# Optimization experiments

Measured on AMD Instinct MI355X. Metric: run time of the kernel, lower is better.

The kernel has to match this reference:

```python
import jax, jax.numpy as jnp
import numpy as np

N = 8192
IN_DIM = 128
THETA_DIM = 256
OUT_DIM = 64
BN_EPS = 1e-5
LEAKY_SLOPE = 0.01


def setup_inputs() -> dict:
    key = jax.random.key(0)
    ks = jax.random.split(key, 8)
    H = jax.random.normal(ks[0], (N, IN_DIM), dtype=jnp.float32)
    # fixed adjacency passed to __init__; nonnegative so mask=ceil(A*1e-5) is {0,1}
    A = jax.random.uniform(ks[1], (N, N), dtype=jnp.float32)
    bn_gamma = jnp.ones((IN_DIM,), dtype=jnp.float32)
    bn_beta = jnp.zeros((IN_DIM,), dtype=jnp.float32)
    W1 = jax.random.normal(ks[2], (IN_DIM, THETA_DIM), dtype=jnp.float32) / np.sqrt(IN_DIM)
    b1 = jnp.zeros((THETA_DIM,), dtype=jnp.float32)
    Wout = jax.random.normal(ks[3], (IN_DIM, OUT_DIM), dtype=jnp.float32) / np.sqrt(IN_DIM)
    bout = jnp.zeros((OUT_DIM,), dtype=jnp.float32)
    return {"H": H, "A": A, "bn_gamma": bn_gamma, "bn_beta": bn_beta,
            "W1": W1, "b1": b1, "Wout": Wout, "bout": bout}


def reference(H, A, bn_gamma, bn_beta, W1, b1, Wout, bout):
    # BatchNorm1d in training mode: batch stats over the N (node) axis, biased var
    mean = jnp.mean(H, axis=0)
    var = jnp.mean(jnp.square(H - mean), axis=0)
    Hn = (H - mean) * jax.lax.rsqrt(var + BN_EPS) * bn_gamma + bn_beta  # [N, IN_DIM]

    Hx = Hn @ W1 + b1                                    # [N, THETA_DIM]
    scores = jax.nn.sigmoid(Hx @ Hx.T)                   # [N, N]
    mask = jnp.ceil(A * 1e-5)                            # binary mask from fixed A
    n = A.shape[0]
    A1 = jnp.maximum(scores, 0.1) * mask + jnp.eye(n, dtype=H.dtype)  # [N, N]

    # D_hat @ A1 @ D_hat is just symmetric row/col scaling by deg^-0.5
    d = jnp.power(jnp.sum(A1, axis=1), -0.5)             # [N]
    A_hat = A1 * d[:, None] * d[None, :]                 # [N, N]

    out = A_hat @ (Hn @ Wout + bout)                     # [N, OUT_DIM]
    out = jnp.where(out >= 0, out, LEAKY_SLOPE * out)    # LeakyReLU(0.01)
    return out, A1
```

## Files before the change

kernel.cpp:

```cpp
#include <hip/hip_runtime.h>
#include <math.h>

#define NN 8192
#define IN_DIM 128
#define THETA_DIM 256
#define OUT_DIM 64

typedef _Float16 half_t;
typedef _Float16 f16x8 __attribute__((ext_vector_type(8)));
typedef _Float16 f16x4 __attribute__((ext_vector_type(4)));
typedef float f32x4 __attribute__((ext_vector_type(4)));

#define WS_SCALE 0
#define WS_SHIFT 128
#define WS_SUM   256
#define WS_SQ    384
#define WS_ROWSUM 512
#define WS_D     8704
#define WS_HN    16896
#define WS_HX    (WS_HN + NN*IN_DIM)
#define WS_Z     (WS_HX + NN*THETA_DIM)
#define WS_OBUF  (WS_Z + NN*OUT_DIM)
#define WS_ZDHT  (WS_OBUF + NN*OUT_DIM)
#define WS_MASK  (WS_ZDHT + NN*OUT_DIM/2)

__global__ __launch_bounds__(256) void k_zero(float* __restrict__ ws) {
    int b = blockIdx.x, tid = threadIdx.x;
    float4 z = (float4){0.f, 0.f, 0.f, 0.f};
    if (b < 9) {
        int i = b * 256 + tid;
        if (i < 2112) ((float4*)(ws + WS_SUM))[i] = z;
    } else {
        int i = (b - 9) * 256 + tid;
        ((float4*)(ws + WS_OBUF))[i] = z;
    }
}

__global__ __launch_bounds__(256) void k_stats(const float* __restrict__ H, float* __restrict__ ws) {
    int tid = threadIdx.x;
    int c = tid & 127, h = tid >> 7;
    int rb = blockIdx.x * 128;
    float s = 0.f, q = 0.f;
    for (int r = h; r < 128; r += 2) {
        float v = H[(size_t)(rb + r) * IN_DIM + c];
        s += v; q += v * v;
    }
    atomicAdd(&ws[WS_SUM + c], s);
    atomicAdd(&ws[WS_SQ + c], q);
}

__global__ void k_finalize(const float* __restrict__ gamma, const float* __restrict__ beta, float* __restrict__ ws) {
    int c = threadIdx.x;
    float mean = ws[WS_SUM + c] * (1.f / NN);
    float var  = ws[WS_SQ + c] * (1.f / NN) - mean * mean;
    float rstd = 1.f / sqrtf(var + 1e-5f);
    float sc = rstd * gamma[c];
    ws[WS_SCALE + c] = sc;
    ws[WS_SHIFT + c] = beta[c] - mean * sc;
}

__global__ __launch_bounds__(256) void k_hn(const float* __restrict__ H, const float* __restrict__ ws, float* __restrict__ Hn) {
    int i = blockIdx.x * 256 + threadIdx.x;
    const float4* H4 = (const float4*)H;
    float4 v = H4[i];
    int cb = (i & 31) * 4;
    float4 sc = *(const float4*)&ws[WS_SCALE + cb];
    float4 sh = *(const float4*)&ws[WS_SHIFT + cb];
    float4 o;
    o.x = v.x * sc.x + sh.x; o.y = v.y * sc.y + sh.y;
    o.z = v.z * sc.z + sh.z; o.w = v.w * sc.w + sh.w;
    ((float4*)Hn)[i] = o;
}

__global__ __launch_bounds__(256) void k_mask(const float* __restrict__ Amat, unsigned int* __restrict__ mask) {
    int idx = blockIdx.x * 256 + threadIdx.x;
    const float4* A4 = (const float4*)Amat;
#pragma unroll
    for (int it = 0; it < 4; it++) {
        int g = idx + it * 524288;
        unsigned int bits = 0u;
#pragma unroll
        for (int w = 0; w < 8; w++) {
            float4 a = A4[(size_t)g * 8 + w];
            bits |= (a.x > 0.f ? 1u : 0u) << (w * 4 + 0);
            bits |= (a.y > 0.f ? 1u : 0u) << (w * 4 + 1);
            bits |= (a.z > 0.f ? 1u : 0u) << (w * 4 + 2);
            bits |= (a.w > 0.f ? 1u : 0u) << (w * 4 + 3);
        }
        mask[g] = bits;
    }
}

__global__ __launch_bounds__(256) void k_hx(const float* __restrict__ Hn, const float* __restrict__ W1,
                                            const float* __restrict__ b1, half_t* __restrict__ Hx) {
    __shared__ float HnS[32 * IN_DIM];
    int tid = threadIdx.x;
    int row0 = blockIdx.x * 32;
    const float4* src = (const float4*)(Hn + (size_t)row0 * IN_DIM);
    float4* dst = (float4*)HnS;
#pragma unroll
    for (int q = 0; q < 4; q++) dst[q * 256 + tid] = src[q * 256 + tid];
    __syncthreads();
    int c = tid;
    float acc[32];
#pragma unroll
    for (int r = 0; r < 32; r++) acc[r] = 0.f;
    for (int k0 = 0; k0 < IN_DIM; k0 += 4) {
        float w0 = W1[(size_t)(k0 + 0) * THETA_DIM + c];
        float w1 = W1[(size_t)(k0 + 1) * THETA_DIM + c];
        float w2 = W1[(size_t)(k0 + 2) * THETA_DIM + c];
        float w3 = W1[(size_t)(k0 + 3) * THETA_DIM + c];
#pragma unroll
        for (int r = 0; r < 32; r++) {
            float4 h = *(const float4*)&HnS[r * IN_DIM + k0];
            acc[r] += h.x * w0 + h.y * w1 + h.z * w2 + h.w * w3;
        }
    }
    float bb = b1[c];
#pragma unroll
    for (int r = 0; r < 32; r++) Hx[(size_t)(row0 + r) * THETA_DIM + c] = (half_t)(acc[r] + bb);
}

__global__ __launch_bounds__(256) void k_y(const float* __restrict__ Hn, const float* __restrict__ Wout,
                                           const float* __restrict__ bout, float* __restrict__ Y) {
    __shared__ float HnS[64 * IN_DIM];
    int tid = threadIdx.x;
    int row0 = blockIdx.x * 64;
    const float4* src = (const float4*)(Hn + (size_t)row0 * IN_DIM);
    float4* dst = (float4*)HnS;
#pragma unroll
    for (int q = 0; q < 8; q++) dst[q * 256 + tid] = src[q * 256 + tid];
    __syncthreads();
    int c = tid & 63, rg = tid >> 6;
    float acc[16];
#pragma unroll
    for (int r = 0; r < 16; r++) acc[r] = 0.f;
    for (int k0 = 0; k0 < IN_DIM; k0 += 4) {
        float w0 = Wout[(size_t)(k0 + 0) * OUT_DIM + c];
        float w1 = Wout[(size_t)(k0 + 1) * OUT_DIM + c];
        float w2 = Wout[(size_t)(k0 + 2) * OUT_DIM + c];
        float w3 = Wout[(size_t)(k0 + 3) * OUT_DIM + c];
#pragma unroll
        for (int r = 0; r < 16; r++) {
            float4 h = *(const float4*)&HnS[(rg * 16 + r) * IN_DIM + k0];
            acc[r] += h.x * w0 + h.y * w1 + h.z * w2 + h.w * w3;
        }
    }
    float bb = bout[c];
#pragma unroll
    for (int r = 0; r < 16; r++) Y[(size_t)(row0 + rg * 16 + r) * OUT_DIM + c] = acc[r] + bb;
}

__global__ __launch_bounds__(256) void k_scores(const half_t* __restrict__ Hx,
                                                const unsigned char* __restrict__ mask,
                                                float* __restrict__ A1, float* __restrict__ rowsum) {
    __shared__ half_t Rs[128 * 72];
    __shared__ half_t Cs[128 * 72];
    int tid = threadIdx.x;
    int R = blockIdx.x * 128, C = blockIdx.y * 128;
    int lane = tid & 63, wv = tid >> 6;
    int li = lane & 15, lg = lane >> 4;
    int qi = (wv >> 1) * 64, qj = (wv & 1) * 64;
    int su = tid & 7;

    f32x4 acc[4][4];
#pragma unroll
    for (int t = 0; t < 4; t++)
#pragma unroll
        for (int u = 0; u < 4; u++) acc[t][u] = (f32x4){0.f, 0.f, 0.f, 0.f};

    f16x8 ra[4], rb[4];
#pragma unroll
    for (int q = 0; q < 4; q++) {
        int r = (q * 256 + tid) >> 3;
        ra[q] = *(const f16x8*)(Hx + (size_t)(R + r) * THETA_DIM + su * 8);
        rb[q] = *(const f16x8*)(Hx + (size_t)(C + r) * THETA_DIM + su * 8);
    }

    for (int s = 0; s < 4; s++) {
        __syncthreads();
#pragma unroll
        for (int q = 0; q < 4; q++) {
            int r = (q * 256 + tid) >> 3;
            *(f16x8*)(Rs + r * 72 + su * 8) = ra[q];
            *(f16x8*)(Cs + r * 72 + su * 8) = rb[q];
        }
        if (s < 3) {
            int k0 = (s + 1) * 64;
#pragma unroll
            for (int q = 0; q < 4; q++) {
                int r = (q * 256 + tid) >> 3;
                ra[q] = *(const f16x8*)(Hx + (size_t)(R + r) * THETA_DIM + k0 + su * 8);
                rb[q] = *(const f16x8*)(Hx + (size_t)(C + r) * THETA_DIM + k0 + su * 8);
            }
        }
        __syncthreads();
#pragma unroll
        for (int kk = 0; kk < 2; kk++) {
            f16x8 af[4], bf[4];
#pragma unroll
            for (int t = 0; t < 4; t++)
                af[t] = *(const f16x8*)(Cs + (qi + t * 16 + li) * 72 + kk * 32 + lg * 8);
#pragma unroll
            for (int u = 0; u < 4; u++)
                bf[u] = *(const f16x8*)(Rs + (qj + u * 16 + li) * 72 + kk * 32 + lg * 8);
#pragma unroll
            for (int t = 0; t < 4; t++)
#pragma unroll
                for (int u = 0; u < 4; u++)
                    acc[t][u] = __builtin_amdgcn_mfma_f32_16x16x32_f16(af[t], bf[u], acc[t][u], 0, 0, 0);
        }
    }

#pragma unroll
    for (int u = 0; u < 4; u++) {
        int gr = R + qj + u * 16 + li;
        unsigned long long m64 = *(const unsigned long long*)&mask[(size_t)gr * 1024 + ((C + qi) >> 3)];
        float rsum = 0.f;
#pragma unroll
        for (int t = 0; t < 4; t++) {
            int gc0 = C + qi + t * 16 + lg * 4;
            float4 wv4;
            float* pv = (float*)&wv4;
#pragma unroll
            for (int jj = 0; jj < 4; jj++) {
                float x = acc[t][u][jj];
                float sg = 1.f / (1.f + __expf(-x));
                float m = (float)((m64 >> (t * 16 + lg * 4 + jj)) & 1ULL);
                float v = fmaxf(sg, 0.1f) * m + ((gr == gc0 + jj) ? 1.f : 0.f);
                pv[jj] = v;
                rsum += v;
            }
            *(float4*)&A1[(size_t)gr * NN + gc0] = wv4;
        }
        rsum += __shfl_xor(rsum, 16, 64);
        rsum += __shfl_xor(rsum, 32, 64);
        if (lg == 0) atomicAdd(&rowsum[gr], rsum);
    }
}

__global__ void k_dvec(float* __restrict__ ws) {
    int i = blockIdx.x * 256 + threadIdx.x;
    ws[WS_D + i] = 1.f / sqrtf(ws[WS_ROWSUM + i]);
}

__global__ __launch_bounds__(256) void k_scalez(const float* __restrict__ dvec, const float* __restrict__ Z,
                                                half_t* __restrict__ ZdhT) {
    __shared__ float T[64 * 68];
    int tid = threadIdx.x;
    int j0 = blockIdx.x * 64;
#pragma unroll
    for (int q = 0; q < 4; q++) {
        int unit = q * 256 + tid;
        int j = unit >> 4, c4 = (unit & 15) * 4;
        float dj = dvec[j0 + j];
        float4 v = *(const float4*)&Z[(size_t)(j0 + j) * OUT_DIM + c4];
        v.x *= dj; v.y *= dj; v.z *= dj; v.w *= dj;
        *(float4*)&T[j * 68 + c4] = v;
    }
    __syncthreads();
#pragma unroll
    for (int q = 0; q < 2; q++) {
        int unit = q * 256 + tid;
        int c = unit >> 3, j8 = (unit & 7) * 8;
        f16x8 h;
#pragma unroll
        for (int x = 0; x < 8; x++) h[x] = (half_t)T[(j8 + x) * 68 + c];
        *(f16x8*)&ZdhT[(size_t)c * NN + j0 + j8] = h;
    }
}

__global__ __launch_bounds__(256) void k_spmm(const float* __restrict__ A1, const half_t* __restrict__ ZdhT,
                                              float* __restrict__ obuf) {
    __shared__ half_t As[128 * 72];
    __shared__ half_t Bs[64 * 72];
    int tid = threadIdx.x;
    int row0 = blockIdx.x * 128;
    int j0 = blockIdx.y * 512;
    int lane = tid & 63, wv = tid >> 6;
    int li = lane & 15, lg = lane >> 4;
    int ar = tid >> 4, ac4 = (tid & 15) * 4;
    int bn = tid >> 3, bk8 = (tid & 7) * 8;

    f32x4 acc[2][4];
#pragma unroll
    for (int t = 0; t < 2; t++)
#pragma unroll
        for (int u = 0; u < 4; u++) acc[t][u] = (f32x4){0.f, 0.f, 0.f, 0.f};

    float4 va[8];
    f16x8 vb[2];
#pragma unroll
    for (int q = 0; q < 8; q++)
        va[q] = *(const float4*)&A1[(size_t)(row0 + (q * 16 + ar)) * NN + j0 + ac4];
#pragma unroll
    for (int q = 0; q < 2; q++)
        vb[q] = *(const f16x8*)&ZdhT[(size_t)(q * 32 + bn) * NN + j0 + bk8];

    for (int jc = j0; jc < j0 + 512; jc += 64) {
        __syncthreads();
#pragma unroll
        for (int q = 0; q < 8; q++) {
            f16x4 h; h[0] = (half_t)va[q].x; h[1] = (half_t)va[q].y; h[2] = (half_t)va[q].z; h[3] = (half_t)va[q].w;
            *(f16x4*)&As[(q * 16 + ar) * 72 + ac4] = h;
        }
#pragma unroll
        for (int q = 0; q < 2; q++)
            *(f16x8*)&Bs[(q * 32 + bn) * 72 + bk8] = vb[q];
        if (jc + 64 < j0 + 512) {
#pragma unroll
            for (int q = 0; q < 8; q++)
                va[q] = *(const float4*)&A1[(size_t)(row0 + (q * 16 + ar)) * NN + jc + 64 + ac4];
#pragma unroll
            for (int q = 0; q < 2; q++)
                vb[q] = *(const f16x8*)&ZdhT[(size_t)(q * 32 + bn) * NN + jc + 64 + bk8];
        }
        __syncthreads();
#pragma unroll
        for (int kk = 0; kk < 2; kk++) {
            f16x8 af[2], bf[4];
#pragma unroll
            for (int t = 0; t < 2; t++)
                af[t] = *(const f16x8*)&As[(wv * 32 + t * 16 + li) * 72 + kk * 32 + lg * 8];
#pragma unroll
            for (int u = 0; u < 4; u++)
                bf[u] = *(const f16x8*)&Bs[(u * 16 + li) * 72 + kk * 32 + lg * 8];
#pragma unroll
            for (int t = 0; t < 2; t++)
#pragma unroll
                for (int u = 0; u < 4; u++)
                    acc[t][u] = __builtin_amdgcn_mfma_f32_16x16x32_f16(af[t], bf[u], acc[t][u], 0, 0, 0);
        }
    }
#pragma unroll
    for (int t = 0; t < 2; t++)
#pragma unroll
        for (int u = 0; u < 4; u++)
#pragma unroll
            for (int r = 0; r < 4; r++)
                atomicAdd(&obuf[(size_t)(row0 + wv * 32 + t * 16 + lg * 4 + r) * OUT_DIM + u * 16 + li],
                          acc[t][u][r]);
}

__global__ void k_out(const float* __restrict__ ws, float* __restrict__ out) {
    int i = blockIdx.x * 256 + threadIdx.x;
    const float4* O4 = (const float4*)(ws + WS_OBUF);
    int row = i >> 4;
    float d = ws[WS_D + row];
    float4 v = O4[i];
    float a = d * v.x, b = d * v.y, cc = d * v.z, e = d * v.w;
    v.x = (a >= 0.f) ? a : 0.01f * a;
    v.y = (b >= 0.f) ? b : 0.01f * b;
    v.z = (cc >= 0.f) ? cc : 0.01f * cc;
    v.w = (e >= 0.f) ? e : 0.01f * e;
    ((float4*)out)[i] = v;
}

extern "C" void kernel_launch(void* const* d_in, const int* in_sizes, int n_in,
                              void* d_out, int out_size, void* d_ws, size_t ws_size,
                              hipStream_t stream) {
    const float* H     = (const float*)d_in[0];
    const float* A     = (const float*)d_in[1];
    const float* gamma = (const float*)d_in[2];
    const float* beta  = (const float*)d_in[3];
    const float* W1    = (const float*)d_in[4];
    const float* b1    = (const float*)d_in[5];
    const float* Wout  = (const float*)d_in[6];
    const float* bout  = (const float*)d_in[7];
    float* out = (float*)d_out;
    float* A1  = out + (size_t)NN * OUT_DIM;
    float* ws  = (float*)d_ws;
    half_t* Hx = (half_t*)(ws + WS_HX);
    half_t* ZdhT = (half_t*)(ws + WS_ZDHT);
    unsigned int* maskw = (unsigned int*)(ws + WS_MASK);

    k_zero<<<521, 256, 0, stream>>>(ws);
    k_mask<<<2048, 256, 0, stream>>>(A, maskw);
    k_stats<<<64, 256, 0, stream>>>(H, ws);
    k_finalize<<<1, 128, 0, stream>>>(gamma, beta, ws);
    k_hn<<<1024, 256, 0, stream>>>(H, ws, ws + WS_HN);
    k_hx<<<256, 256, 0, stream>>>(ws + WS_HN, W1, b1, Hx);
    k_y<<<128, 256, 0, stream>>>(ws + WS_HN, Wout, bout, ws + WS_Z);
    dim3 g6(64, 64);
    k_scores<<<g6, 256, 0, stream>>>(Hx, (const unsigned char*)maskw, A1, ws + WS_ROWSUM);
    k_dvec<<<32, 256, 0, stream>>>(ws);
    k_scalez<<<128, 256, 0, stream>>>(ws + WS_D, ws + WS_Z, ZdhT);
    k_spmm<<<dim3(64, 16), 256, 0, stream>>>(A1, ZdhT, ws + WS_OBUF);
    k_out<<<512, 256, 0, stream>>>(ws, out);
}
```

Baseline: 337.8 us.

## Restructure spmm with direct-register A loads, partial buffers, and nontemporal traffic

k_spmm now loads A1 rows straight into registers in MFMA fragment layout instead of staging them through shared memory, and double-buffers the Z tile in LDS so there is one barrier per step. Its float atomics on the output are replaced by per-split partial buffers that a new output kernel sums before scaling and applying LeakyReLU, so the zeroing of the output buffer is dropped. Nontemporal loads and stores are added for the large A and A1 streams, the mask prefetch in k_scores is hoisted before the main loop, and k_stats gets more blocks. The partial buffers cost extra workspace and extra read traffic in the final kernel.

```diff
diff --git a/kernel.cpp b/kernel.cpp
--- a/kernel.cpp
+++ b/kernel.cpp
@@ -23,25 +23,19 @@
 #define WS_OBUF  (WS_Z + NN*OUT_DIM)
 #define WS_ZDHT  (WS_OBUF + NN*OUT_DIM)
 #define WS_MASK  (WS_ZDHT + NN*OUT_DIM/2)
+#define WS_OBUFP (WS_MASK + NN*(NN/32))
 
 __global__ __launch_bounds__(256) void k_zero(float* __restrict__ ws) {
-    int b = blockIdx.x, tid = threadIdx.x;
-    float4 z = (float4){0.f, 0.f, 0.f, 0.f};
-    if (b < 9) {
-        int i = b * 256 + tid;
-        if (i < 2112) ((float4*)(ws + WS_SUM))[i] = z;
-    } else {
-        int i = (b - 9) * 256 + tid;
-        ((float4*)(ws + WS_OBUF))[i] = z;
-    }
+    int i = blockIdx.x * 256 + threadIdx.x;
+    if (i < 2112) ((float4*)(ws + WS_SUM))[i] = (float4){0.f, 0.f, 0.f, 0.f};
 }
 
 __global__ __launch_bounds__(256) void k_stats(const float* __restrict__ H, float* __restrict__ ws) {
     int tid = threadIdx.x;
     int c = tid & 127, h = tid >> 7;
-    int rb = blockIdx.x * 128;
+    int rb = blockIdx.x * 32;
     float s = 0.f, q = 0.f;
-    for (int r = h; r < 128; r += 2) {
+    for (int r = h; r < 32; r += 2) {
         float v = H[(size_t)(rb + r) * IN_DIM + c];
         s += v; q += v * v;
     }
@@ -74,18 +68,18 @@
 
 __global__ __launch_bounds__(256) void k_mask(const float* __restrict__ Amat, unsigned int* __restrict__ mask) {
     int idx = blockIdx.x * 256 + threadIdx.x;
-    const float4* A4 = (const float4*)Amat;
+    const f32x4* A4 = (const f32x4*)Amat;
 #pragma unroll
     for (int it = 0; it < 4; it++) {
         int g = idx + it * 524288;
         unsigned int bits = 0u;
 #pragma unroll
         for (int w = 0; w < 8; w++) {
-            float4 a = A4[(size_t)g * 8 + w];
-            bits |= (a.x > 0.f ? 1u : 0u) << (w * 4 + 0);
-            bits |= (a.y > 0.f ? 1u : 0u) << (w * 4 + 1);
-            bits |= (a.z > 0.f ? 1u : 0u) << (w * 4 + 2);
-            bits |= (a.w > 0.f ? 1u : 0u) << (w * 4 + 3);
+            f32x4 a = __builtin_nontemporal_load(&A4[(size_t)g * 8 + w]);
+            bits |= (a[0] > 0.f ? 1u : 0u) << (w * 4 + 0);
+            bits |= (a[1] > 0.f ? 1u : 0u) << (w * 4 + 1);
+            bits |= (a[2] > 0.f ? 1u : 0u) << (w * 4 + 2);
+            bits |= (a[3] > 0.f ? 1u : 0u) << (w * 4 + 3);
         }
         mask[g] = bits;
     }
@@ -176,6 +170,12 @@
         ra[q] = *(const f16x8*)(Hx + (size_t)(R + r) * THETA_DIM + su * 8);
         rb[q] = *(const f16x8*)(Hx + (size_t)(C + r) * THETA_DIM + su * 8);
     }
+    unsigned long long m64p[4];
+#pragma unroll
+    for (int u = 0; u < 4; u++) {
+        int gr = R + qj + u * 16 + li;
+        m64p[u] = *(const unsigned long long*)&mask[(size_t)gr * 1024 + ((C + qi) >> 3)];
+    }
 
     for (int s = 0; s < 4; s++) {
         __syncthreads();
@@ -215,23 +215,22 @@
 #pragma unroll
     for (int u = 0; u < 4; u++) {
         int gr = R + qj + u * 16 + li;
-        unsigned long long m64 = *(const unsigned long long*)&mask[(size_t)gr * 1024 + ((C + qi) >> 3)];
+        unsigned long long m64 = m64p[u];
         float rsum = 0.f;
 #pragma unroll
         for (int t = 0; t < 4; t++) {
             int gc0 = C + qi + t * 16 + lg * 4;
-            float4 wv4;
-            float* pv = (float*)&wv4;
+            f32x4 wv4;
 #pragma unroll
             for (int jj = 0; jj < 4; jj++) {
                 float x = acc[t][u][jj];
                 float sg = 1.f / (1.f + __expf(-x));
                 float m = (float)((m64 >> (t * 16 + lg * 4 + jj)) & 1ULL);
                 float v = fmaxf(sg, 0.1f) * m + ((gr == gc0 + jj) ? 1.f : 0.f);
-                pv[jj] = v;
+                wv4[jj] = v;
                 rsum += v;
             }
-            *(float4*)&A1[(size_t)gr * NN + gc0] = wv4;
+            __builtin_nontemporal_store(wv4, (f32x4*)&A1[(size_t)gr * NN + gc0]);
         }
         rsum += __shfl_xor(rsum, 16, 64);
         rsum += __shfl_xor(rsum, 32, 64);
@@ -271,15 +270,13 @@
 }
 
 __global__ __launch_bounds__(256) void k_spmm(const float* __restrict__ A1, const half_t* __restrict__ ZdhT,
-                                              float* __restrict__ obuf) {
-    __shared__ half_t As[128 * 72];
-    __shared__ half_t Bs[64 * 72];
+                                              float* __restrict__ obufP) {
+    __shared__ half_t Bs[2][64 * 72];
     int tid = threadIdx.x;
     int row0 = blockIdx.x * 128;
     int j0 = blockIdx.y * 512;
     int lane = tid & 63, wv = tid >> 6;
     int li = lane & 15, lg = lane >> 4;
-    int ar = tid >> 4, ac4 = (tid & 15) * 4;
     int bn = tid >> 3, bk8 = (tid & 7) * 8;
 
     f32x4 acc[2][4];
@@ -288,67 +285,95 @@
 #pragma unroll
         for (int u = 0; u < 4; u++) acc[t][u] = (f32x4){0.f, 0.f, 0.f, 0.f};
 
-    float4 va[8];
     f16x8 vb[2];
-#pragma unroll
-    for (int q = 0; q < 8; q++)
-        va[q] = *(const float4*)&A1[(size_t)(row0 + (q * 16 + ar)) * NN + j0 + ac4];
 #pragma unroll
     for (int q = 0; q < 2; q++)
         vb[q] = *(const f16x8*)&ZdhT[(size_t)(q * 32 + bn) * NN + j0 + bk8];
-
-    for (int jc = j0; jc < j0 + 512; jc += 64) {
+    f32x4 a_raw[4][2];
+#pragma unroll
+    for (int t = 0; t < 2; t++)
+#pragma unroll
+        for (int kk = 0; kk < 2; kk++) {
+            const float* p = &A1[(size_t)(row0 + wv * 32 + t * 16 + li) * NN + j0 + kk * 32 + lg * 8];
+            a_raw[t * 2 + kk][0] = __builtin_nontemporal_load((const f32x4*)p);
+            a_raw[t * 2 + kk][1] = __builtin_nontemporal_load((const f32x4*)(p + 4));
+        }
+#pragma unroll
+    for (int q = 0; q < 2; q++)
+        *(f16x8*)&Bs[0][(q * 32 + bn) * 72 + bk8] = vb[q];
+    __syncthreads();
+
+    for (int s = 0; s < 8; s++) {
+        int cur = s & 1;
+        int jn = j0 + (s + 1) * 64;
+        if (s < 7) {
+#pragma unroll
+            for (int q = 0; q < 2; q++)
+                vb[q] = *(const f16x8*)&ZdhT[(size_t)(q * 32 + bn) * NN + jn + bk8];
+        }
+        f16x8 af[2][2];
+#pragma unroll
+        for (int t = 0; t < 2; t++)
+#pragma unroll
+            for (int kk = 0; kk < 2; kk++) {
+                f32x4 a0 = a_raw[t * 2 + kk][0], a1 = a_raw[t * 2 + kk][1];
+                f16x8 h;
+                h[0] = (half_t)a0[0]; h[1] = (half_t)a0[1]; h[2] = (half_t)a0[2]; h[3] = (half_t)a0[3];
+                h[4] = (half_t)a1[0]; h[5] = (half_t)a1[1]; h[6] = (half_t)a1[2]; h[7] = (half_t)a1[3];
+                af[t][kk] = h;
+            }
+        if (s < 7) {
+#pragma unroll
+            for (int t = 0; t < 2; t++)
+#pragma unroll
+                for (int kk = 0; kk < 2; kk++) {
+                    const float* p = &A1[(size_t)(row0 + wv * 32 + t * 16 + li) * NN + jn + kk * 32 + lg * 8];
+                    a_raw[t * 2 + kk][0] = __builtin_nontemporal_load((const f32x4*)p);
+                    a_raw[t * 2 + kk][1] = __builtin_nontemporal_load((const f32x4*)(p + 4));
+                }
+        }
+#pragma unroll
+        for (int kk = 0; kk < 2; kk++) {
+            f16x8 bf[4];
+#pragma unroll
+            for (int u = 0; u < 4; u++)
+                bf[u] = *(const f16x8*)&Bs[cur][(u * 16 + li) * 72 + kk * 32 + lg * 8];
+#pragma unroll
+            for (int t = 0; t < 2; t++)
+#pragma unroll
+                for (int u = 0; u < 4; u++)
+                    acc[t][u] = __builtin_amdgcn_mfma_f32_16x16x32_f16(af[t][kk], bf[u], acc[t][u], 0, 0, 0);
+        }
+        if (s < 7) {
+#pragma unroll
+            for (int q = 0; q < 2; q++)
+                *(f16x8*)&Bs[cur ^ 1][(q * 32 + bn) * 72 + bk8] = vb[q];
+        }
         __syncthreads();
-#pragma unroll
-        for (int q = 0; q < 8; q++) {
-            f16x4 h; h[0] = (half_t)va[q].x; h[1] = (half_t)va[q].y; h[2] = (half_t)va[q].z; h[3] = (half_t)va[q].w;
-            *(f16x4*)&As[(q * 16 + ar) * 72 + ac4] = h;
-        }
-#pragma unroll
-        for (int q = 0; q < 2; q++)
-            *(f16x8*)&Bs[(q * 32 + bn) * 72 + bk8] = vb[q];
-        if (jc + 64 < j0 + 512) {
-#pragma unroll
-            for (int q = 0; q < 8; q++)
-                va[q] = *(const float4*)&A1[(size_t)(row0 + (q * 16 + ar)) * NN + jc + 64 + ac4];
-#pragma unroll
-            for (int q = 0; q < 2; q++)
-                vb[q] = *(const f16x8*)&ZdhT[(size_t)(q * 32 + bn) * NN + jc + 64 + bk8];
-        }
-        __syncthreads();
-#pragma unroll
-        for (int kk = 0; kk < 2; kk++) {
-            f16x8 af[2], bf[4];
-#pragma unroll
-            for (int t = 0; t < 2; t++)
-                af[t] = *(const f16x8*)&As[(wv * 32 + t * 16 + li) * 72 + kk * 32 + lg * 8];
-#pragma unroll
-            for (int u = 0; u < 4; u++)
-                bf[u] = *(const f16x8*)&Bs[(u * 16 + li) * 72 + kk * 32 + lg * 8];
-#pragma unroll
-            for (int t = 0; t < 2; t++)
-#pragma unroll
-                for (int u = 0; u < 4; u++)
-                    acc[t][u] = __builtin_amdgcn_mfma_f32_16x16x32_f16(af[t], bf[u], acc[t][u], 0, 0, 0);
-        }
-    }
+    }
+    float* P = obufP + (size_t)blockIdx.y * NN * OUT_DIM;
 #pragma unroll
     for (int t = 0; t < 2; t++)
 #pragma unroll
         for (int u = 0; u < 4; u++)
 #pragma unroll
             for (int r = 0; r < 4; r++)
-                atomicAdd(&obuf[(size_t)(row0 + wv * 32 + t * 16 + lg * 4 + r) * OUT_DIM + u * 16 + li],
-                          acc[t][u][r]);
-}
-
-__global__ void k_out(const float* __restrict__ ws, float* __restrict__ out) {
+                P[(size_t)(row0 + wv * 32 + t * 16 + lg * 4 + r) * OUT_DIM + u * 16 + li] = acc[t][u][r];
+}
+
+__global__ void k_out_p(const float* __restrict__ ws, float* __restrict__ out) {
     int i = blockIdx.x * 256 + threadIdx.x;
-    const float4* O4 = (const float4*)(ws + WS_OBUF);
+    const float4* P = (const float4*)(ws + WS_OBUFP);
+    float4 s = P[i];
+#pragma unroll
+    for (int p = 1; p < 16; p++) {
+        float4 v = P[(size_t)p * 131072 + i];
+        s.x += v.x; s.y += v.y; s.z += v.z; s.w += v.w;
+    }
     int row = i >> 4;
     float d = ws[WS_D + row];
-    float4 v = O4[i];
-    float a = d * v.x, b = d * v.y, cc = d * v.z, e = d * v.w;
+    float a = d * s.x, b = d * s.y, cc = d * s.z, e = d * s.w;
+    float4 v;
     v.x = (a >= 0.f) ? a : 0.01f * a;
     v.y = (b >= 0.f) ? b : 0.01f * b;
     v.z = (cc >= 0.f) ? cc : 0.01f * cc;
@@ -374,9 +399,9 @@
     half_t* ZdhT = (half_t*)(ws + WS_ZDHT);
     unsigned int* maskw = (unsigned int*)(ws + WS_MASK);
 
-    k_zero<<<521, 256, 0, stream>>>(ws);
+    k_zero<<<9, 256, 0, stream>>>(ws);
     k_mask<<<2048, 256, 0, stream>>>(A, maskw);
-    k_stats<<<64, 256, 0, stream>>>(H, ws);
+    k_stats<<<256, 256, 0, stream>>>(H, ws);
     k_finalize<<<1, 128, 0, stream>>>(gamma, beta, ws);
     k_hn<<<1024, 256, 0, stream>>>(H, ws, ws + WS_HN);
     k_hx<<<256, 256, 0, stream>>>(ws + WS_HN, W1, b1, Hx);
@@ -385,6 +410,6 @@
     k_scores<<<g6, 256, 0, stream>>>(Hx, (const unsigned char*)maskw, A1, ws + WS_ROWSUM);
     k_dvec<<<32, 256, 0, stream>>>(ws);
     k_scalez<<<128, 256, 0, stream>>>(ws + WS_D, ws + WS_Z, ZdhT);
-    k_spmm<<<dim3(64, 16), 256, 0, stream>>>(A1, ZdhT, ws + WS_OBUF);
-    k_out<<<512, 256, 0, stream>>>(ws, out);
-}
+    k_spmm<<<dim3(64, 16), 256, 0, stream>>>(A1, ZdhT, ws + WS_OBUFP);
+    k_out_p<<<512, 256, 0, stream>>>(ws, out);
+}
```

After: 397.7 us. +17.7%, slower.

## Replace spmm atomics with per-split partial buffers and tune several small kernels

Applied to the files above, without the earlier changes.

Each K-split block of the spmm now writes its tile to its own partial output buffer instead of doing atomicAdd into one shared buffer. A final kernel sums the 16 partials, then applies the degree scaling and LeakyReLU, which also removes the need to zero the output buffer. Several smaller edits ride along: nontemporal loads of A in the mask kernel, the mask word in the scores kernel loaded before the main loop, and more, smaller blocks for the BN statistics. The partial buffers cost extra workspace and extra write/read traffic (16 x 2 MB), and the MFMA operand gets an odd `af*0+af` expression that should compile away.

```diff
diff --git a/kernel.cpp b/kernel.cpp
--- a/kernel.cpp
+++ b/kernel.cpp
@@ -23,25 +23,19 @@
 #define WS_OBUF  (WS_Z + NN*OUT_DIM)
 #define WS_ZDHT  (WS_OBUF + NN*OUT_DIM)
 #define WS_MASK  (WS_ZDHT + NN*OUT_DIM/2)
+#define WS_OBUFP (WS_MASK + NN*(NN/32))
 
 __global__ __launch_bounds__(256) void k_zero(float* __restrict__ ws) {
-    int b = blockIdx.x, tid = threadIdx.x;
-    float4 z = (float4){0.f, 0.f, 0.f, 0.f};
-    if (b < 9) {
-        int i = b * 256 + tid;
-        if (i < 2112) ((float4*)(ws + WS_SUM))[i] = z;
-    } else {
-        int i = (b - 9) * 256 + tid;
-        ((float4*)(ws + WS_OBUF))[i] = z;
-    }
+    int i = blockIdx.x * 256 + threadIdx.x;
+    if (i < 2112) ((float4*)(ws + WS_SUM))[i] = (float4){0.f, 0.f, 0.f, 0.f};
 }
 
 __global__ __launch_bounds__(256) void k_stats(const float* __restrict__ H, float* __restrict__ ws) {
     int tid = threadIdx.x;
     int c = tid & 127, h = tid >> 7;
-    int rb = blockIdx.x * 128;
+    int rb = blockIdx.x * 32;
     float s = 0.f, q = 0.f;
-    for (int r = h; r < 128; r += 2) {
+    for (int r = h; r < 32; r += 2) {
         float v = H[(size_t)(rb + r) * IN_DIM + c];
         s += v; q += v * v;
     }
@@ -74,18 +68,18 @@
 
 __global__ __launch_bounds__(256) void k_mask(const float* __restrict__ Amat, unsigned int* __restrict__ mask) {
     int idx = blockIdx.x * 256 + threadIdx.x;
-    const float4* A4 = (const float4*)Amat;
+    const f32x4* A4 = (const f32x4*)Amat;
 #pragma unroll
     for (int it = 0; it < 4; it++) {
         int g = idx + it * 524288;
         unsigned int bits = 0u;
 #pragma unroll
         for (int w = 0; w < 8; w++) {
-            float4 a = A4[(size_t)g * 8 + w];
-            bits |= (a.x > 0.f ? 1u : 0u) << (w * 4 + 0);
-            bits |= (a.y > 0.f ? 1u : 0u) << (w * 4 + 1);
-            bits |= (a.z > 0.f ? 1u : 0u) << (w * 4 + 2);
-            bits |= (a.w > 0.f ? 1u : 0u) << (w * 4 + 3);
+            f32x4 a = __builtin_nontemporal_load(&A4[(size_t)g * 8 + w]);
+            bits |= (a[0] > 0.f ? 1u : 0u) << (w * 4 + 0);
+            bits |= (a[1] > 0.f ? 1u : 0u) << (w * 4 + 1);
+            bits |= (a[2] > 0.f ? 1u : 0u) << (w * 4 + 2);
+            bits |= (a[3] > 0.f ? 1u : 0u) << (w * 4 + 3);
         }
         mask[g] = bits;
     }
@@ -176,6 +170,12 @@
         ra[q] = *(const f16x8*)(Hx + (size_t)(R + r) * THETA_DIM + su * 8);
         rb[q] = *(const f16x8*)(Hx + (size_t)(C + r) * THETA_DIM + su * 8);
     }
+    unsigned long long m64p[4];
+#pragma unroll
+    for (int u = 0; u < 4; u++) {
+        int gr = R + qj + u * 16 + li;
+        m64p[u] = *(const unsigned long long*)&mask[(size_t)gr * 1024 + ((C + qi) >> 3)];
+    }
 
     for (int s = 0; s < 4; s++) {
         __syncthreads();
@@ -215,7 +215,7 @@
 #pragma unroll
     for (int u = 0; u < 4; u++) {
         int gr = R + qj + u * 16 + li;
-        unsigned long long m64 = *(const unsigned long long*)&mask[(size_t)gr * 1024 + ((C + qi) >> 3)];
+        unsigned long long m64 = m64p[u];
         float rsum = 0.f;
 #pragma unroll
         for (int t = 0; t < 4; t++) {
@@ -271,7 +271,7 @@
 }
 
 __global__ __launch_bounds__(256) void k_spmm(const float* __restrict__ A1, const half_t* __restrict__ ZdhT,
-                                              float* __restrict__ obuf) {
+                                              float* __restrict__ obufP) {
     __shared__ half_t As[128 * 72];
     __shared__ half_t Bs[64 * 72];
     int tid = threadIdx.x;
@@ -329,26 +329,32 @@
             for (int t = 0; t < 2; t++)
 #pragma unroll
                 for (int u = 0; u < 4; u++)
-                    acc[t][u] = __builtin_amdgcn_mfma_f32_16x16x32_f16(af[t], bf[u], acc[t][u], 0, 0, 0);
-        }
-    }
+                    acc[t][u] = __builtin_amdgcn_mfma_f32_16x16x32_f16(af[t][0] * 0 + af[t], bf[u], acc[t][u], 0, 0, 0);
+        }
+    }
+    float* P = obufP + (size_t)blockIdx.y * NN * OUT_DIM;
 #pragma unroll
     for (int t = 0; t < 2; t++)
 #pragma unroll
         for (int u = 0; u < 4; u++)
 #pragma unroll
             for (int r = 0; r < 4; r++)
-                atomicAdd(&obuf[(size_t)(row0 + wv * 32 + t * 16 + lg * 4 + r) * OUT_DIM + u * 16 + li],
-                          acc[t][u][r]);
-}
-
-__global__ void k_out(const float* __restrict__ ws, float* __restrict__ out) {
+                P[(size_t)(row0 + wv * 32 + t * 16 + lg * 4 + r) * OUT_DIM + u * 16 + li] = acc[t][u][r];
+}
+
+__global__ void k_out_p(const float* __restrict__ ws, float* __restrict__ out) {
     int i = blockIdx.x * 256 + threadIdx.x;
-    const float4* O4 = (const float4*)(ws + WS_OBUF);
+    const float4* P = (const float4*)(ws + WS_OBUFP);
+    float4 s = P[i];
+#pragma unroll
+    for (int p = 1; p < 16; p++) {
+        float4 v = P[(size_t)p * 131072 + i];
+        s.x += v.x; s.y += v.y; s.z += v.z; s.w += v.w;
+    }
     int row = i >> 4;
     float d = ws[WS_D + row];
-    float4 v = O4[i];
-    float a = d * v.x, b = d * v.y, cc = d * v.z, e = d * v.w;
+    float a = d * s.x, b = d * s.y, cc = d * s.z, e = d * s.w;
+    float4 v;
     v.x = (a >= 0.f) ? a : 0.01f * a;
     v.y = (b >= 0.f) ? b : 0.01f * b;
     v.z = (cc >= 0.f) ? cc : 0.01f * cc;
@@ -374,9 +380,9 @@
     half_t* ZdhT = (half_t*)(ws + WS_ZDHT);
     unsigned int* maskw = (unsigned int*)(ws + WS_MASK);
 
-    k_zero<<<521, 256, 0, stream>>>(ws);
+    k_zero<<<9, 256, 0, stream>>>(ws);
     k_mask<<<2048, 256, 0, stream>>>(A, maskw);
-    k_stats<<<64, 256, 0, stream>>>(H, ws);
+    k_stats<<<256, 256, 0, stream>>>(H, ws);
     k_finalize<<<1, 128, 0, stream>>>(gamma, beta, ws);
     k_hn<<<1024, 256, 0, stream>>>(H, ws, ws + WS_HN);
     k_hx<<<256, 256, 0, stream>>>(ws + WS_HN, W1, b1, Hx);
@@ -385,6 +391,6 @@
     k_scores<<<g6, 256, 0, stream>>>(Hx, (const unsigned char*)maskw, A1, ws + WS_ROWSUM);
     k_dvec<<<32, 256, 0, stream>>>(ws);
     k_scalez<<<128, 256, 0, stream>>>(ws + WS_D, ws + WS_Z, ZdhT);
-    k_spmm<<<dim3(64, 16), 256, 0, stream>>>(A1, ZdhT, ws + WS_OBUF);
-    k_out<<<512, 256, 0, stream>>>(ws, out);
-}
+    k_spmm<<<dim3(64, 16), 256, 0, stream>>>(A1, ZdhT, ws + WS_OBUFP);
+    k_out_p<<<512, 256, 0, stream>>>(ws, out);
+}
```

Result: slower. 410.7 us (+21.6%).
